# Performance work log

Measured on AMD Instinct MI355X. Metric: run time of the kernel, lower is better.

## Reference

```python
import jax, jax.numpy as jnp
import numpy as np
from jax import lax

B, N, K, M, NC = 64, 1024, 20, 256, 40  # clouds, points/cloud, knn k, fps points (ratio 0.25), classes
EPS = 1e-5


def setup_inputs() -> dict:
    key = jax.random.key(0)
    ks = jax.random.split(key, 6)
    w = lambda k, s: jax.random.normal(k, s, jnp.float32) * 0.05
    return {
        "pos": jax.random.normal(ks[0], (B * N, 3), jnp.float32),
        "w1": w(ks[1], (64, 3)), "b1": jnp.zeros(64, jnp.float32),
        "g1": jnp.ones(64, jnp.float32), "be1": jnp.zeros(64, jnp.float32),
        "w2": w(ks[2], (64, 64)), "b2": jnp.zeros(64, jnp.float32),
        "g2": jnp.ones(64, jnp.float32), "be2": jnp.zeros(64, jnp.float32),
        "w_nn1": w(ks[3], (512, 64)), "b_nn1": jnp.zeros(512, jnp.float32),
        "g_bn2": jnp.ones(512, jnp.float32), "be_bn2": jnp.zeros(512, jnp.float32),
        "w_nn4": w(ks[4], (NC, 512)), "b_nn4": jnp.zeros(NC, jnp.float32),
    }


def _knn_idx(p):  # p: [N,3] -> [N,K] neighbor indices, self excluded (loop=False)
    d = jnp.sum(p * p, -1)[:, None] + jnp.sum(p * p, -1)[None, :] - 2.0 * (p @ p.T)
    d = d.at[jnp.arange(N), jnp.arange(N)].set(jnp.inf)
    _, idx = lax.top_k(-d, K)
    return idx


def _fps_idx(p):  # p: [N,3] -> [M] farthest-point-sampling indices (deterministic start at 0)
    def step(carry, _):
        dist, last = carry
        d = jnp.sum((p - p[last]) ** 2, -1)
        dist = jnp.minimum(dist, d)
        nxt = jnp.argmax(dist).astype(jnp.int32)
        return (dist, nxt), nxt
    init = (jnp.full((N,), 1e38, jnp.float32), jnp.int32(0))
    _, idxs = lax.scan(step, init, None, length=M - 1)
    return jnp.concatenate([jnp.zeros((1,), jnp.int32), idxs])


def _bn(x, g, b, axes):  # batch-norm with batch statistics (training mode)
    m = jnp.mean(x, axes, keepdims=True)
    v = jnp.var(x, axes, keepdims=True)
    return (x - m) * lax.rsqrt(v + EPS) * g + b


def reference(pos, w1, b1, g1, be1, w2, b2, g2, be2,
              w_nn1, b_nn1, g_bn2, be_bn2, w_nn4, b_nn4):
    p = pos.reshape(B, N, 3)
    idx = jax.vmap(_knn_idx)(p)                     # [B,N,K]
    nbr = jax.vmap(lambda pb, ib: pb[ib])(p, idx)   # [B,N,K,3]
    rel = nbr - p[:, :, None, :]                    # edge features (relative positions)
    h = jax.nn.relu(jnp.einsum('bnkc,fc->bnkf', rel, w1) + b1)
    h = _bn(h, g1, be1, (0, 1, 2))
    h = jax.nn.relu(jnp.einsum('bnkf,gf->bnkg', h, w2) + b2)
    h = _bn(h, g2, be2, (0, 1, 2))
    feat = jnp.max(h, axis=2)                       # [B,N,64] edge-conv max aggregation
    fidx = jax.vmap(_fps_idx)(p)                    # [B,M]
    f = jnp.take_along_axis(feat, fidx[:, :, None], axis=1)  # [B,M,64]
    y = jnp.einsum('bmf,hf->bmh', f, w_nn1) + b_nn1  # [B,M,512]
    y = jnp.max(y, axis=1)                           # [B,512]
    y = jax.nn.relu(y)
    y = _bn(y, g_bn2, be_bn2, (0,))
    y = y @ w_nn4.T + b_nn4                          # [B,40]
    return jax.nn.log_softmax(y, axis=1)
```

## Files before the change

### kernel.cpp

```cpp
#include <hip/hip_runtime.h>
#include <hip/hip_bf16.h>
#include <cfloat>
#include <math.h>

#define BB 64
#define NN 1024
#define KNN 20
#define MM 256
#define CC 64
#define HH 512
#define NCLS 40
#define EPSF 1e-5f
#define CNT1 (BB*NN*KNN)

#define FPS_R1 131
#define FPS_R2 176

#define IDX_OFF    0
#define MAXH2_OFF  (IDX_OFF + BB*NN*KNN)
#define FIDX_OFF   (MAXH2_OFF + BB*NN*CC)
#define Y_OFF      (FIDX_OFF + BB*MM)
#define ACC_OFF    (Y_OFF + BB*HH)
#define W2T_OFF    (ACC_OFF + 256)
#define B2F_OFF    (W2T_OFF + CC*CC)
#define FPSD_OFF   (B2F_OFF + CC)
#define FPSC_OFF   (FPSD_OFF + BB*NN)

typedef __attribute__((ext_vector_type(8)))  short short8;
typedef __attribute__((ext_vector_type(16))) float f32x16;

static __device__ __forceinline__ unsigned short f2bf(float f) {
  unsigned u = __float_as_uint(f);
  unsigned r = (u + 0x7fffu + ((u >> 16) & 1u)) >> 16;
  return (unsigned short)r;
}

static __device__ __forceinline__ void fps_phase(
    const float* sx, const float* sy, const float* sz,
    float* fpsd, int* fpsc, int* fidxg, int b, int mStart, int mEnd) {
  int lane = threadIdx.x;
  float lx[16], ly[16], lz[16], dist[16];
#pragma unroll
  for (int q = 0; q < 16; ++q) {
    int j = q*64 + lane;
    lx[q] = sx[j]; ly[q] = sy[j]; lz[q] = sz[j];
  }
  int cur;
  if (mStart <= 1) {
#pragma unroll
    for (int q = 0; q < 16; ++q) dist[q] = 1e38f;
    if (lane == 0) fidxg[b*MM] = 0;
    cur = 0;
  } else {
#pragma unroll
    for (int q = 0; q < 16; ++q) dist[q] = fpsd[b*NN + q*64 + lane];
    cur = fpsc[b];
  }
  for (int m = mStart; m < mEnd; ++m) {
    float cpx = sx[cur], cpy = sy[cur], cpz = sz[cur];
#pragma unroll
    for (int q = 0; q < 16; ++q) {
      float dx = __fsub_rn(lx[q], cpx);
      float dy = __fsub_rn(ly[q], cpy);
      float dz = __fsub_rn(lz[q], cpz);
      float dd = __fadd_rn(__fadd_rn(__fmul_rn(dx,dx), __fmul_rn(dy,dy)), __fmul_rn(dz,dz));
      dist[q] = fminf(dist[q], dd);
    }
    float t8[8];
#pragma unroll
    for (int q = 0; q < 8; ++q) t8[q] = fmaxf(dist[q], dist[q + 8]);
#pragma unroll
    for (int q = 0; q < 4; ++q) t8[q] = fmaxf(t8[q], t8[q + 4]);
    float r = fmaxf(fmaxf(t8[0], t8[1]), fmaxf(t8[2], t8[3]));
#define FPS_VMAX_STEP(C) { \
    int tt = __builtin_amdgcn_update_dpp(__float_as_int(r), __float_as_int(r), (C), 0xf, 0xf, false); \
    r = fmaxf(r, __int_as_float(tt)); }
    FPS_VMAX_STEP(0x111)
    FPS_VMAX_STEP(0x112)
    FPS_VMAX_STEP(0x114)
    FPS_VMAX_STEP(0x118)
    FPS_VMAX_STEP(0x142)
    FPS_VMAX_STEP(0x143)
#undef FPS_VMAX_STEP
    float wmax = __int_as_float(__builtin_amdgcn_readlane(__float_as_int(r), 63));
    unsigned ci = 0xFFFFFFFFu;
#pragma unroll
    for (int q = 15; q >= 0; --q)
      if (dist[q] == wmax) ci = (unsigned)(q*64 + lane);
#define FPS_IMIN_STEP(C) { \
    unsigned tt = (unsigned)__builtin_amdgcn_update_dpp((int)ci, (int)ci, (C), 0xf, 0xf, false); \
    ci = (tt < ci) ? tt : ci; }
    FPS_IMIN_STEP(0x111)
    FPS_IMIN_STEP(0x112)
    FPS_IMIN_STEP(0x114)
    FPS_IMIN_STEP(0x118)
    FPS_IMIN_STEP(0x142)
    FPS_IMIN_STEP(0x143)
#undef FPS_IMIN_STEP
    cur = (int)(unsigned)__builtin_amdgcn_readlane((int)ci, 63);
    if (lane == 0) fidxg[b*MM + m] = cur;
  }
  if (mEnd < MM) {
#pragma unroll
    for (int q = 0; q < 16; ++q) fpsd[b*NN + q*64 + lane] = dist[q];
    if (lane == 0) fpsc[b] = cur;
  }
}

__global__ __launch_bounds__(256) void knn_fps_kernel(const float* __restrict__ pos,
                                                      int* __restrict__ idxg,
                                                      int* __restrict__ fidxg,
                                                      float* __restrict__ fpsd,
                                                      int* __restrict__ fpsc) {
  __shared__ float4 pj[NN];
  if (blockIdx.x >= BB) {
    int blk = blockIdx.x - BB;
    int b  = blk >> 5;
    int nb = blk & 31;
    const float* pb = pos + (size_t)b * NN * 3;
    for (int i = threadIdx.x; i < NN; i += 256) {
      float x = pb[i*3+0], y = pb[i*3+1], z = pb[i*3+2];
      pj[i] = make_float4(x, y, z, (x*x + y*y) + z*z);
    }
    __syncthreads();
    int lane = threadIdx.x & 63;
    int wv   = threadIdx.x >> 6;
    unsigned long long lmask_lt = (1ULL << lane) - 1ULL;

    for (int t = 0; t < 8; ++t) {
      int i = nb*32 + wv*8 + t;
      float4 pi = pj[i];
      unsigned u[16];
#pragma unroll
      for (int q = 0; q < 16; ++q) {
        int j = q*64 + lane;
        float4 pw = pj[j];
        float d = pi.w + pw.w - 2.0f*(pi.x*pw.x + pi.y*pw.y + pi.z*pw.z);
        unsigned bits = __float_as_uint(d);
        bits = (bits & 0x80000000u) ? ~bits : (bits | 0x80000000u);
        if (j == i) bits = 0xFFFFFFFFu;
        u[q] = bits;
      }
      unsigned lmin = u[0];
#pragma unroll
      for (int q = 1; q < 16; ++q) lmin = (u[q] < lmin) ? u[q] : lmin;
      unsigned rmin = lmin, rmax = lmin;
#define KNN_DPP_STEP(C) { \
      unsigned t1 = (unsigned)__builtin_amdgcn_update_dpp((int)rmin, (int)rmin, (C), 0xf, 0xf, false); \
      unsigned t2 = (unsigned)__builtin_amdgcn_update_dpp((int)rmax, (int)rmax, (C), 0xf, 0xf, false); \
      rmin = (t1 < rmin) ? t1 : rmin; rmax = (t2 > rmax) ? t2 : rmax; }
      KNN_DPP_STEP(0x111)
      KNN_DPP_STEP(0x112)
      KNN_DPP_STEP(0x114)
      KNN_DPP_STEP(0x118)
      KNN_DPP_STEP(0x142)
      KNN_DPP_STEP(0x143)
#undef KNN_DPP_STEP
      unsigned plo = ((unsigned)__builtin_amdgcn_readlane((int)rmin, 63)) >> 16;
      unsigned phi = ((unsigned)__builtin_amdgcn_readlane((int)rmax, 63)) >> 16;
      int cntHi = -1;
      while (plo < phi) {
        unsigned pmid = (plo + phi) >> 1;
        unsigned tmid = (pmid << 16) | 0xFFFFu;
        int cnt = 0;
#pragma unroll
        for (int q = 0; q < 16; ++q)
          cnt += (int)__popcll(__ballot(u[q] <= tmid));
        if (cnt >= KNN) { phi = pmid; cntHi = cnt; } else plo = pmid + 1;
      }
      unsigned tstar = (phi << 16) | 0xFFFFu;
      unsigned bbase = phi << 16;
      int* op = idxg + (size_t)(b*NN + i) * KNN;
      if (cntHi < 0) {
        cntHi = 0;
#pragma unroll
        for (int q = 0; q < 16; ++q)
          cntHi += (int)__popcll(__ballot(u[q] <= tstar));
      }
      if (cntHi == KNN) {
        int base = 0;
#pragma unroll
        for (int q = 0; q < 16; ++q) {
          bool pred = (u[q] <= tstar);
          unsigned long long mask = __ballot((int)pred);
          if (pred) op[base + (int)__popcll(mask & lmask_lt)] = q*64 + lane;
          base += (int)__popcll(mask);
        }
      } else {
        unsigned lo2 = bbase, hi2 = tstar;
        while (lo2 < hi2) {
          unsigned mid = lo2 + ((hi2 - lo2) >> 1);
          int cnt = 0;
#pragma unroll
          for (int q = 0; q < 16; ++q)
            cnt += (int)__popcll(__ballot(u[q] <= mid));
          if (cnt >= KNN) hi2 = mid; else lo2 = mid + 1;
        }
        unsigned xstar = lo2;
        int base = 0;
#pragma unroll
        for (int q = 0; q < 16; ++q) {
          bool pred = (u[q] < xstar);
          unsigned long long mask = __ballot((int)pred);
          if (pred) op[base + (int)__popcll(mask & lmask_lt)] = q*64 + lane;
          base += (int)__popcll(mask);
        }
        for (int q = 0; q < 16 && base < KNN; ++q) {
          bool pred = (u[q] == xstar);
          unsigned long long mask = __ballot((int)pred);
          if (pred) {
            int pos_ = base + (int)__popcll(mask & lmask_lt);
            if (pos_ < KNN) op[pos_] = q*64 + lane;
          }
          base += (int)__popcll(mask);
        }
      }
    }
  } else {
    int b = blockIdx.x;
    float* base = (float*)pj;
    float* sx = base; float* sy = base + NN; float* sz = base + 2*NN;
    const float* pb = pos + (size_t)b * NN * 3;
    for (int i = threadIdx.x; i < NN; i += 256) {
      sx[i] = pb[i*3+0]; sy[i] = pb[i*3+1]; sz[i] = pb[i*3+2];
    }
    __syncthreads();
    if (threadIdx.x >= 64) return;
    fps_phase(sx, sy, sz, fpsd, fpsc, fidxg, b, 1, FPS_R1);
  }
}

__global__ __launch_bounds__(256) void stats1_kernel(const float* __restrict__ pos,
    const int* __restrict__ idxg, const float* __restrict__ w1,
    const float* __restrict__ b1, float* __restrict__ acc,
    int* __restrict__ fidxg, float* __restrict__ fpsd, int* __restrict__ fpsc) {
  __shared__ float px[NN], py[NN], pz[NN];
  __shared__ float relx[4][KNN], rely[4][KNN], relz[4][KNN];
  __shared__ float red[4][CC];
  if (blockIdx.x < BB) {
    int b = blockIdx.x;
    const float* pb = pos + (size_t)b*NN*3;
    for (int i = threadIdx.x; i < NN; i += 256) {
      px[i] = pb[i*3+0]; py[i] = pb[i*3+1]; pz[i] = pb[i*3+2];
    }
    __syncthreads();
    if (threadIdx.x >= 64) return;
    fps_phase(px, py, pz, fpsd, fpsc, fidxg, b, FPS_R1, FPS_R2);
    return;
  }
  int blk = blockIdx.x - BB;
  int b = blk >> 4;
  int nb = blk & 15;
  const float* pb = pos + (size_t)b*NN*3;
  for (int i = threadIdx.x; i < NN; i += 256) {
    px[i] = pb[i*3+0]; py[i] = pb[i*3+1]; pz[i] = pb[i*3+2];
  }
  int c = threadIdx.x & 63, w = threadIdx.x >> 6;
  float w1x = w1[c*3+0], w1y = w1[c*3+1], w1z = w1[c*3+2], b1c = b1[c];
  float s = 0.f, ss = 0.f;
  __syncthreads();
  for (int it = 0; it < 16; ++it) {
    int n0 = nb*64 + it*4;
    if (threadIdx.x < 80) {
      int wv = threadIdx.x / KNN, k = threadIdx.x % KNN;
      int n = n0 + wv;
      int j = idxg[(size_t)(b*NN + n)*KNN + k];
      relx[wv][k] = px[j] - px[n];
      rely[wv][k] = py[j] - py[n];
      relz[wv][k] = pz[j] - pz[n];
    }
    __syncthreads();
#pragma unroll
    for (int k = 0; k < KNN; ++k) {
      float h = fmaxf(relx[w][k]*w1x + rely[w][k]*w1y + relz[w][k]*w1z + b1c, 0.f);
      s += h; ss += h*h;
    }
    __syncthreads();
  }
  red[w][c] = s; __syncthreads();
  if (w == 0) atomicAdd(&acc[c], red[0][c]+red[1][c]+red[2][c]+red[3][c]);
  __syncthreads();
  red[w][c] = ss; __syncthreads();
  if (w == 0) atomicAdd(&acc[64+c], red[0][c]+red[1][c]+red[2][c]+red[3][c]);
}

__global__ void fold1_kernel(const float* __restrict__ acc, const float* __restrict__ g1,
    const float* __restrict__ be1, const float* __restrict__ w2, const float* __restrict__ b2,
    unsigned short* __restrict__ w2bf, float* __restrict__ b2f) {
  __shared__ float s1[CC], t1[CC];
  int tid = threadIdx.x;
  if (tid < CC) {
    float cnt = (float)CNT1;
    float m = acc[tid] / cnt;
    float v = acc[64+tid] / cnt - m*m;
    float sc = g1[tid] * rsqrtf(v + EPSF);
    s1[tid] = sc; t1[tid] = be1[tid] - m*sc;
  }
  __syncthreads();
  int frag = tid >> 6;
  int lane = tid & 63;
  int nt = frag >> 2, ks = frag & 3;
  int cout = nt*32 + (lane & 31);
  int cin0 = ks*16 + (lane >> 5)*8;
  for (int j = 0; j < 8; ++j) {
    int cin = cin0 + j;
    w2bf[((size_t)frag*64 + lane)*8 + j] = f2bf(w2[cout*CC + cin] * s1[cin]);
  }
  if (tid < CC) {
    float accb = b2[tid];
    for (int ci = 0; ci < CC; ++ci) accb += t1[ci]*w2[tid*CC + ci];
    b2f[tid] = accb;
  }
}

__global__ __launch_bounds__(256, 4) void conv2_kernel(const float* __restrict__ pos,
    const int* __restrict__ idxg, const float* __restrict__ w1, const float* __restrict__ b1,
    const unsigned short* __restrict__ w2bf, const float* __restrict__ b2fg,
    float* __restrict__ maxh2, float* __restrict__ acc2,
    int* __restrict__ fidxg, float* __restrict__ fpsd, int* __restrict__ fpsc) {
  __shared__ float px[NN], py[NN], pz[NN];
  __shared__ float4 relw[4][KNN];
  __shared__ __align__(16) unsigned short h1s[4][2112];
  __shared__ float redbuf[4][2*CC];
  if (blockIdx.x < BB) {
    int b = blockIdx.x;
    const float* pb = pos + (size_t)b*NN*3;
    for (int i = threadIdx.x; i < NN; i += 256) {
      px[i] = pb[i*3+0]; py[i] = pb[i*3+1]; pz[i] = pb[i*3+2];
    }
    __syncthreads();
    if (threadIdx.x >= 64) return;
    fps_phase(px, py, pz, fpsd, fpsc, fidxg, b, FPS_R2, MM);
    return;
  }
  int blk = blockIdx.x - BB;
  int b = blk >> 4;
  int nb = blk & 15;
  const float* pb = pos + (size_t)b*NN*3;
  for (int i = threadIdx.x; i < NN; i += 256) {
    px[i] = pb[i*3+0]; py[i] = pb[i*3+1]; pz[i] = pb[i*3+2];
  }
  int lane = threadIdx.x & 63, w = threadIdx.x >> 6;
  int half = lane >> 5, l31 = lane & 31;
  short8 Bf[2][4];
#pragma unroll
  for (int nt = 0; nt < 2; ++nt)
#pragma unroll
    for (int ks = 0; ks < 4; ++ks)
      Bf[nt][ks] = *(const short8*)&w2bf[((size_t)(nt*4+ks)*64 + lane)*8];
  float b2o0 = b2fg[l31], b2o1 = b2fg[32 + l31];
  float w1x = w1[lane*3+0], w1y = w1[lane*3+1], w1z = w1[lane*3+2], b1c = b1[lane];
  unsigned short* hw = h1s[w];
  {
    short8 zz = {0,0,0,0,0,0,0,0};
    for (int z = lane; z < 96; z += 64) {
      int g = z / 12, r = 20 + z % 12;
      *(short8*)&hw[g*264 + r*8] = zz;
    }
  }
  float sA = 0.f, ssA = 0.f, sB = 0.f, ssB = 0.f;
  __syncthreads();
  for (int t = 0; t < 16; ++t) {
    int n = nb*64 + w*16 + t;
    if (lane < KNN) {
      int j = idxg[(size_t)(b*NN + n)*KNN + lane];
      relw[w][lane] = make_float4(px[j]-px[n], py[j]-py[n], pz[j]-pz[n], 0.f);
    }
    int gbase = (lane >> 3)*264 + (lane & 7);
#pragma unroll
    for (int k = 0; k < KNN; ++k) {
      float4 r4 = relw[w][k];
      float h = fmaxf(fmaf(r4.x, w1x, fmaf(r4.y, w1y, fmaf(r4.z, w1z, b1c))), 0.f);
      hw[gbase + k*8] = f2bf(h);
    }
    f32x16 acc0 = {}; f32x16 acc1 = {};
#pragma unroll
    for (int ks = 0; ks < 4; ++ks) {
      short8 A = *(const short8*)&hw[(ks*2 + half)*264 + l31*8];
      acc0 = __builtin_amdgcn_mfma_f32_32x32x16_bf16(A, Bf[0][ks], acc0, 0, 0, 0);
      acc1 = __builtin_amdgcn_mfma_f32_32x32x16_bf16(A, Bf[1][ks], acc1, 0, 0, 0);
    }
    float mx0 = 0.f, mx1 = 0.f;
#pragma unroll
    for (int reg = 0; reg < 8; ++reg) {
      float v0 = fmaxf(acc0[reg] + b2o0, 0.f);
      float v1 = fmaxf(acc1[reg] + b2o1, 0.f);
      sA += v0; ssA += v0*v0; sB += v1; ssB += v1*v1;
      mx0 = fmaxf(mx0, v0); mx1 = fmaxf(mx1, v1);
    }
    if (half == 0) {
#pragma unroll
      for (int reg = 8; reg < 12; ++reg) {
        float v0 = fmaxf(acc0[reg] + b2o0, 0.f);
        float v1 = fmaxf(acc1[reg] + b2o1, 0.f);
        sA += v0; ssA += v0*v0; sB += v1; ssB += v1*v1;
        mx0 = fmaxf(mx0, v0); mx1 = fmaxf(mx1, v1);
      }
    }
    mx0 = fmaxf(mx0, __shfl_xor(mx0, 32, 64));
    mx1 = fmaxf(mx1, __shfl_xor(mx1, 32, 64));
    if (half == 0) {
      float* mp = maxh2 + (size_t)(b*NN + n)*CC;
      mp[l31] = mx0; mp[32 + l31] = mx1;
    }
  }
  sA += __shfl_xor(sA, 32, 64); ssA += __shfl_xor(ssA, 32, 64);
  sB += __shfl_xor(sB, 32, 64); ssB += __shfl_xor(ssB, 32, 64);
  if (half == 0) { redbuf[w][l31] = sA; redbuf[w][32 + l31] = sB; }
  __syncthreads();
  if (w == 0) atomicAdd(&acc2[lane], redbuf[0][lane]+redbuf[1][lane]+redbuf[2][lane]+redbuf[3][lane]);
  __syncthreads();
  if (half == 0) { redbuf[w][l31] = ssA; redbuf[w][32 + l31] = ssB; }
  __syncthreads();
  if (w == 0) atomicAdd(&acc2[64+lane], redbuf[0][lane]+redbuf[1][lane]+redbuf[2][lane]+redbuf[3][lane]);
}

__global__ __launch_bounds__(256) void head_kernel(const float* __restrict__ maxh2,
    const int* __restrict__ fidxg, const float* __restrict__ acc2,
    const float* __restrict__ g2, const float* __restrict__ be2,
    const float* __restrict__ wnn1, const float* __restrict__ bnn1, float* __restrict__ Y) {
  int b = blockIdx.x >> 2;
  int hc = blockIdx.x & 3;
  __shared__ __align__(16) float ftile[128][CC];
  __shared__ float red2[4][128];
  __shared__ float s2s[CC], t2s[CC];
  if (threadIdx.x < CC) {
    int c = threadIdx.x;
    float cnt = (float)CNT1;
    float m = acc2[c]/cnt;
    float v = acc2[64+c]/cnt - m*m;
    float sc = g2[c]*rsqrtf(v+EPSF);
    s2s[c] = sc;
    t2s[c] = be2[c] - m*sc;
  }
  int hl = threadIdx.x & 63, mseg = threadIdx.x >> 6;
  int hA = hc*128 + hl, hB = hA + 64;
  float4 wva[16], wvb[16];
  const float4* wrA = (const float4*)(wnn1 + (size_t)hA*CC);
  const float4* wrB = (const float4*)(wnn1 + (size_t)hB*CC);
#pragma unroll
  for (int q = 0; q < 16; ++q) { wva[q] = wrA[q]; wvb[q] = wrB[q]; }
  float bestA = -FLT_MAX, bestB = -FLT_MAX;
  const int* fb = fidxg + b*MM;
  __syncthreads();
  for (int chunk = 0; chunk < 2; ++chunk) {
    {
      int row = threadIdx.x & 127, chal = threadIdx.x >> 7;
      int fi = fb[chunk*128 + row];
      const float* src = maxh2 + (size_t)(b*NN + fi)*CC;
      for (int ci = chal*32; ci < chal*32+32; ++ci)
        ftile[row][ci] = s2s[ci]*src[ci] + t2s[ci];
    }
    __syncthreads();
    for (int m = mseg*32; m < mseg*32+32; ++m) {
      float accA = 0.f, accB = 0.f;
#pragma unroll
      for (int cq = 0; cq < 16; ++cq) {
        float4 f = *((const float4*)&ftile[m][cq*4]);
        accA = fmaf(f.x, wva[cq].x, accA);
        accA = fmaf(f.y, wva[cq].y, accA);
        accA = fmaf(f.z, wva[cq].z, accA);
        accA = fmaf(f.w, wva[cq].w, accA);
        accB = fmaf(f.x, wvb[cq].x, accB);
        accB = fmaf(f.y, wvb[cq].y, accB);
        accB = fmaf(f.z, wvb[cq].z, accB);
        accB = fmaf(f.w, wvb[cq].w, accB);
      }
      bestA = fmaxf(bestA, accA);
      bestB = fmaxf(bestB, accB);
    }
    __syncthreads();
  }
  red2[mseg][hl] = bestA;
  red2[mseg][64 + hl] = bestB;
  __syncthreads();
  if (threadIdx.x < 128) {
    int hh = hc*128 + threadIdx.x;
    float v = fmaxf(fmaxf(red2[0][threadIdx.x], red2[1][threadIdx.x]),
                    fmaxf(red2[2][threadIdx.x], red2[3][threadIdx.x])) + bnn1[hh];
    Y[(size_t)b*HH + hh] = fmaxf(v, 0.f);
  }
}

__global__ __launch_bounds__(256) void logits_kernel(const float* __restrict__ Y,
    const float* __restrict__ g3, const float* __restrict__ be3,
    const float* __restrict__ w4, const float* __restrict__ b4, float* __restrict__ out) {
  int b = blockIdx.x;
  __shared__ float ybn[HH];
  __shared__ float s3s[HH], t3s[HH];
  __shared__ float lg[NCLS];
  __shared__ float lse;
  for (int h = threadIdx.x; h < HH; h += 256) {
    float s = 0.f;
    for (int bb = 0; bb < BB; ++bb) s += Y[(size_t)bb*HH + h];
    float m = s / (float)BB;
    float v = 0.f;
    for (int bb = 0; bb < BB; ++bb) { float d = Y[(size_t)bb*HH + h] - m; v += d*d; }
    v /= (float)BB;
    float sc = g3[h] * rsqrtf(v + EPSF);
    s3s[h] = sc; t3s[h] = be3[h] - m*sc;
  }
  __syncthreads();
  for (int hh = threadIdx.x; hh < HH; hh += 256)
    ybn[hh] = Y[(size_t)b*HH + hh]*s3s[hh] + t3s[hh];
  __syncthreads();
  if (threadIdx.x < NCLS) {
    int j = threadIdx.x;
    float acc = b4[j];
    const float* wr = w4 + (size_t)j*HH;
    for (int ci = 0; ci < HH; ++ci) acc = fmaf(ybn[ci], wr[ci], acc);
    lg[j] = acc;
  }
  __syncthreads();
  if (threadIdx.x == 0) {
    float mx = -FLT_MAX;
    for (int j = 0; j < NCLS; ++j) mx = fmaxf(mx, lg[j]);
    float s = 0.f;
    for (int j = 0; j < NCLS; ++j) s += expf(lg[j] - mx);
    lse = mx + logf(s);
  }
  __syncthreads();
  if (threadIdx.x < NCLS) out[b*NCLS + threadIdx.x] = lg[threadIdx.x] - lse;
}

extern "C" void kernel_launch(void* const* d_in, const int* in_sizes, int n_in,
                              void* d_out, int out_size, void* d_ws, size_t ws_size,
                              hipStream_t stream) {
  const float* pos  = (const float*)d_in[0];
  const float* w1   = (const float*)d_in[1];
  const float* b1   = (const float*)d_in[2];
  const float* g1   = (const float*)d_in[3];
  const float* be1  = (const float*)d_in[4];
  const float* w2   = (const float*)d_in[5];
  const float* b2   = (const float*)d_in[6];
  const float* g2   = (const float*)d_in[7];
  const float* be2  = (const float*)d_in[8];
  const float* wnn1 = (const float*)d_in[9];
  const float* bnn1 = (const float*)d_in[10];
  const float* gbn2 = (const float*)d_in[11];
  const float* bebn2= (const float*)d_in[12];
  const float* wnn4 = (const float*)d_in[13];
  const float* bnn4 = (const float*)d_in[14];
  float* ws = (float*)d_ws;
  int*   idxg  = (int*)(ws + IDX_OFF);
  float* maxh2 = ws + MAXH2_OFF;
  int*   fidxg = (int*)(ws + FIDX_OFF);
  float* Y     = ws + Y_OFF;
  float* acc1  = ws + ACC_OFF;
  float* acc2  = ws + ACC_OFF + 128;
  unsigned short* w2bf = (unsigned short*)(ws + W2T_OFF);
  float* b2f   = ws + B2F_OFF;
  float* fpsd  = ws + FPSD_OFF;
  int*   fpsc  = (int*)(ws + FPSC_OFF);
  float* outp  = (float*)d_out;

  hipMemsetAsync((void*)(ws + ACC_OFF), 0, 256*sizeof(float), stream);
  knn_fps_kernel<<<BB + BB*32, 256, 0, stream>>>(pos, idxg, fidxg, fpsd, fpsc);
  stats1_kernel<<<BB + BB*16, 256, 0, stream>>>(pos, idxg, w1, b1, acc1, fidxg, fpsd, fpsc);
  fold1_kernel<<<1, 512, 0, stream>>>(acc1, g1, be1, w2, b2, w2bf, b2f);
  conv2_kernel<<<BB + BB*16, 256, 0, stream>>>(pos, idxg, w1, b1, w2bf, b2f, maxh2, acc2, fidxg, fpsd, fpsc);
  head_kernel<<<BB*4, 256, 0, stream>>>(maxh2, fidxg, acc2, g2, be2, wnn1, bnn1, Y);
  logits_kernel<<<BB, 256, 0, stream>>>(Y, gbn2, bebn2, wnn4, bnn4, outp);
}
```

Baseline: 352.6 us.

## Fuse first-layer BN statistics into kNN kernel and rebalance FPS split

Removes the separate stats1 kernel by computing the conv1 ReLU sum and sum-of-squares inside the kNN blocks, right after each point's neighbours are selected, using a small shared-memory neighbour list. This avoids a kernel launch, re-reading the index array from global memory, and reloading positions. The FPS work that ran concurrently in stats1 is redistributed, so FPS now runs in two phases (1..201 and 201..256) overlapped with the kNN and conv2 kernels instead of three. The risk is that a longer FPS phase in the kNN kernel becomes the critical path, and that the extra per-point work lengthens the kNN blocks.

```diff
diff --git a/kernel.cpp b/kernel.cpp
--- a/kernel.cpp
+++ b/kernel.cpp
@@ -13,8 +13,7 @@
 #define EPSF 1e-5f
 #define CNT1 (BB*NN*KNN)
 
-#define FPS_R1 131
-#define FPS_R2 176
+#define FPS_R1 201
 
 #define IDX_OFF    0
 #define MAXH2_OFF  (IDX_OFF + BB*NN*KNN)
@@ -111,8 +110,13 @@
                                                       int* __restrict__ idxg,
                                                       int* __restrict__ fidxg,
                                                       float* __restrict__ fpsd,
-                                                      int* __restrict__ fpsc) {
+                                                      int* __restrict__ fpsc,
+                                                      const float* __restrict__ w1,
+                                                      const float* __restrict__ b1,
+                                                      float* __restrict__ acc1) {
   __shared__ float4 pj[NN];
+  __shared__ int nbrs[4][KNN];
+  __shared__ float red[4][CC];
   if (blockIdx.x >= BB) {
     int blk = blockIdx.x - BB;
     int b  = blk >> 5;
@@ -126,6 +130,8 @@
     int lane = threadIdx.x & 63;
     int wv   = threadIdx.x >> 6;
     unsigned long long lmask_lt = (1ULL << lane) - 1ULL;
+    float w1x = w1[lane*3+0], w1y = w1[lane*3+1], w1z = w1[lane*3+2], b1c = b1[lane];
+    float s = 0.f, ss = 0.f;
 
     for (int t = 0; t < 8; ++t) {
       int i = nb*32 + wv*8 + t;
@@ -183,7 +189,11 @@
         for (int q = 0; q < 16; ++q) {
           bool pred = (u[q] <= tstar);
           unsigned long long mask = __ballot((int)pred);
-          if (pred) op[base + (int)__popcll(mask & lmask_lt)] = q*64 + lane;
+          if (pred) {
+            int p_ = base + (int)__popcll(mask & lmask_lt);
+            op[p_] = q*64 + lane;
+            nbrs[wv][p_] = q*64 + lane;
+          }
           base += (int)__popcll(mask);
         }
       } else {
@@ -202,20 +212,38 @@
         for (int q = 0; q < 16; ++q) {
           bool pred = (u[q] < xstar);
           unsigned long long mask = __ballot((int)pred);
-          if (pred) op[base + (int)__popcll(mask & lmask_lt)] = q*64 + lane;
+          if (pred) {
+            int p_ = base + (int)__popcll(mask & lmask_lt);
+            op[p_] = q*64 + lane;
+            nbrs[wv][p_] = q*64 + lane;
+          }
           base += (int)__popcll(mask);
         }
         for (int q = 0; q < 16 && base < KNN; ++q) {
           bool pred = (u[q] == xstar);
           unsigned long long mask = __ballot((int)pred);
           if (pred) {
-            int pos_ = base + (int)__popcll(mask & lmask_lt);
-            if (pos_ < KNN) op[pos_] = q*64 + lane;
+            int p_ = base + (int)__popcll(mask & lmask_lt);
+            if (p_ < KNN) { op[p_] = q*64 + lane; nbrs[wv][p_] = q*64 + lane; }
           }
           base += (int)__popcll(mask);
         }
       }
-    }
+#pragma unroll 4
+      for (int k = 0; k < KNN; ++k) {
+        int j = nbrs[wv][k];
+        float4 pw = pj[j];
+        float h = fmaxf(fmaf(pw.x - pi.x, w1x,
+                       fmaf(pw.y - pi.y, w1y,
+                       fmaf(pw.z - pi.z, w1z, b1c))), 0.f);
+        s += h; ss += h*h;
+      }
+    }
+    red[wv][lane] = s; __syncthreads();
+    if (wv == 0) atomicAdd(&acc1[lane], red[0][lane]+red[1][lane]+red[2][lane]+red[3][lane]);
+    __syncthreads();
+    red[wv][lane] = ss; __syncthreads();
+    if (wv == 0) atomicAdd(&acc1[64+lane], red[0][lane]+red[1][lane]+red[2][lane]+red[3][lane]);
   } else {
     int b = blockIdx.x;
     float* base = (float*)pj;
@@ -228,60 +256,6 @@
     if (threadIdx.x >= 64) return;
     fps_phase(sx, sy, sz, fpsd, fpsc, fidxg, b, 1, FPS_R1);
   }
-}
-
-__global__ __launch_bounds__(256) void stats1_kernel(const float* __restrict__ pos,
-    const int* __restrict__ idxg, const float* __restrict__ w1,
-    const float* __restrict__ b1, float* __restrict__ acc,
-    int* __restrict__ fidxg, float* __restrict__ fpsd, int* __restrict__ fpsc) {
-  __shared__ float px[NN], py[NN], pz[NN];
-  __shared__ float relx[4][KNN], rely[4][KNN], relz[4][KNN];
-  __shared__ float red[4][CC];
-  if (blockIdx.x < BB) {
-    int b = blockIdx.x;
-    const float* pb = pos + (size_t)b*NN*3;
-    for (int i = threadIdx.x; i < NN; i += 256) {
-      px[i] = pb[i*3+0]; py[i] = pb[i*3+1]; pz[i] = pb[i*3+2];
-    }
-    __syncthreads();
-    if (threadIdx.x >= 64) return;
-    fps_phase(px, py, pz, fpsd, fpsc, fidxg, b, FPS_R1, FPS_R2);
-    return;
-  }
-  int blk = blockIdx.x - BB;
-  int b = blk >> 4;
-  int nb = blk & 15;
-  const float* pb = pos + (size_t)b*NN*3;
-  for (int i = threadIdx.x; i < NN; i += 256) {
-    px[i] = pb[i*3+0]; py[i] = pb[i*3+1]; pz[i] = pb[i*3+2];
-  }
-  int c = threadIdx.x & 63, w = threadIdx.x >> 6;
-  float w1x = w1[c*3+0], w1y = w1[c*3+1], w1z = w1[c*3+2], b1c = b1[c];
-  float s = 0.f, ss = 0.f;
-  __syncthreads();
-  for (int it = 0; it < 16; ++it) {
-    int n0 = nb*64 + it*4;
-    if (threadIdx.x < 80) {
-      int wv = threadIdx.x / KNN, k = threadIdx.x % KNN;
-      int n = n0 + wv;
-      int j = idxg[(size_t)(b*NN + n)*KNN + k];
-      relx[wv][k] = px[j] - px[n];
-      rely[wv][k] = py[j] - py[n];
-      relz[wv][k] = pz[j] - pz[n];
-    }
-    __syncthreads();
-#pragma unroll
-    for (int k = 0; k < KNN; ++k) {
-      float h = fmaxf(relx[w][k]*w1x + rely[w][k]*w1y + relz[w][k]*w1z + b1c, 0.f);
-      s += h; ss += h*h;
-    }
-    __syncthreads();
-  }
-  red[w][c] = s; __syncthreads();
-  if (w == 0) atomicAdd(&acc[c], red[0][c]+red[1][c]+red[2][c]+red[3][c]);
-  __syncthreads();
-  red[w][c] = ss; __syncthreads();
-  if (w == 0) atomicAdd(&acc[64+c], red[0][c]+red[1][c]+red[2][c]+red[3][c]);
 }
 
 __global__ void fold1_kernel(const float* __restrict__ acc, const float* __restrict__ g1,
@@ -330,7 +304,7 @@
     }
     __syncthreads();
     if (threadIdx.x >= 64) return;
-    fps_phase(px, py, pz, fpsd, fpsc, fidxg, b, FPS_R2, MM);
+    fps_phase(px, py, pz, fpsd, fpsc, fidxg, b, FPS_R1, MM);
     return;
   }
   int blk = blockIdx.x - BB;
@@ -555,8 +529,7 @@
   float* outp  = (float*)d_out;
 
   hipMemsetAsync((void*)(ws + ACC_OFF), 0, 256*sizeof(float), stream);
-  knn_fps_kernel<<<BB + BB*32, 256, 0, stream>>>(pos, idxg, fidxg, fpsd, fpsc);
-  stats1_kernel<<<BB + BB*16, 256, 0, stream>>>(pos, idxg, w1, b1, acc1, fidxg, fpsd, fpsc);
+  knn_fps_kernel<<<BB + BB*32, 256, 0, stream>>>(pos, idxg, fidxg, fpsd, fpsc, w1, b1, acc1);
   fold1_kernel<<<1, 512, 0, stream>>>(acc1, g1, be1, w2, b2, w2bf, b2f);
   conv2_kernel<<<BB + BB*16, 256, 0, stream>>>(pos, idxg, w1, b1, w2bf, b2f, maxh2, acc2, fidxg, fpsd, fpsc);
   head_kernel<<<BB*4, 256, 0, stream>>>(maxh2, fidxg, acc2, g2, be2, wnn1, bnn1, Y);
```

New measurement: 336.2 us. 4.7% less time.
